# Kernel optimization log

Hardware: AMD Instinct MI355X
Metric: run time of the kernel (lower is better)

The kernel has to match this reference:

```python
import jax, jax.numpy as jnp
import numpy as np

B, L, D_MODEL = 2, 1024, 1024
EXPAND = 2
D_INNER = EXPAND * D_MODEL      # 2048
D_STATE = 16
D_CONV = 4
DT_RANK = D_MODEL // 16         # 64


def setup_inputs() -> dict:
    key = jax.random.key(0)
    ks = jax.random.split(key, 8)
    s = 0.02
    x = jax.random.normal(ks[0], (B, L, D_MODEL), jnp.float32)
    W_in = (jax.random.normal(ks[1], (D_MODEL, 2 * D_INNER), jnp.float32) * s)
    conv_w = jax.random.normal(ks[2], (D_INNER, 1, D_CONV), jnp.float32) * 0.2  # depthwise kernel (O,I/g,K)
    conv_b = jnp.zeros((D_INNER,), jnp.float32)
    W_xproj = jax.random.normal(ks[3], (D_INNER, DT_RANK + 2 * D_STATE), jnp.float32) * s
    W_dt = jax.random.normal(ks[4], (DT_RANK, D_INNER), jnp.float32) * (DT_RANK ** -0.5)
    b_dt = jnp.full((D_INNER,), -4.6, jnp.float32)  # softplus^{-1}(~0.01), mamba-style dt init
    A_log = jnp.log(jnp.broadcast_to(jnp.arange(1, D_STATE + 1, dtype=jnp.float32), (D_INNER, D_STATE)))
    D_skip = jnp.ones((D_INNER,), jnp.float32)
    W_out = jax.random.normal(ks[5], (D_INNER, D_MODEL), jnp.float32) * s
    return dict(x=x, W_in=W_in, conv_w=conv_w, conv_b=conv_b, W_xproj=W_xproj,
                W_dt=W_dt, b_dt=b_dt, A_log=A_log, D_skip=D_skip, W_out=W_out)


def _mamba(x, W_in, conv_w, conv_b, W_xproj, W_dt, b_dt, A_log, D_skip, W_out):
    b, l, _ = x.shape
    # input projection and gate split
    xz = jnp.einsum('bld,de->ble', x, W_in)            # (B, L, 2*d_inner)
    x_in, z = jnp.split(xz, 2, axis=-1)                # each (B, L, d_inner)
    # causal depthwise conv1d + SiLU
    xt = jnp.transpose(x_in, (0, 2, 1))                # (B, d_inner, L)
    xt = jnp.pad(xt, ((0, 0), (0, 0), (D_CONV - 1, 0)))
    conv = jax.lax.conv_general_dilated(
        xt, conv_w, window_strides=(1,), padding='VALID',
        dimension_numbers=('NCH', 'OIH', 'NCH'), feature_group_count=D_INNER)
    conv = conv + conv_b[None, :, None]                # (B, d_inner, L)
    u = jax.nn.silu(jnp.transpose(conv, (0, 2, 1)))    # (B, L, d_inner)
    # input-dependent SSM parameters
    x_dbl = jnp.einsum('bld,de->ble', u, W_xproj)      # (B, L, dt_rank + 2*d_state)
    dt_lr = x_dbl[..., :DT_RANK]
    Bm = x_dbl[..., DT_RANK:DT_RANK + D_STATE]         # (B, L, d_state)
    Cm = x_dbl[..., DT_RANK + D_STATE:]                # (B, L, d_state)
    delta = jax.nn.softplus(jnp.einsum('blr,rd->bld', dt_lr, W_dt) + b_dt)  # (B, L, d_inner)
    A = -jnp.exp(A_log)                                # (d_inner, d_state)
    dA = jnp.exp(jnp.einsum('bld,dn->bldn', delta, A))           # (B, L, d_inner, d_state)
    dBu = (delta * u)[..., None] * Bm[:, :, None, :]              # (B, L, d_inner, d_state)
    # selective scan over time
    def step(h, inp):
        dA_t, dBu_t, C_t = inp
        h = dA_t * h + dBu_t                           # (B, d_inner, d_state)
        y_t = jnp.einsum('bdn,bn->bd', h, C_t)
        return h, y_t
    h0 = jnp.zeros((b, D_INNER, D_STATE), x.dtype)
    _, ys = jax.lax.scan(step, h0, (jnp.swapaxes(dA, 0, 1), jnp.swapaxes(dBu, 0, 1), jnp.swapaxes(Cm, 0, 1)))
    y = jnp.swapaxes(ys, 0, 1)                          # (B, L, d_inner)
    y = y + D_skip * u
    y = y * jax.nn.silu(z)
    out = jnp.einsum('bld,de->ble', y, W_out)           # (B, L, d_model)
    return out  # dropout is identity in eval mode


def reference(x, W_in, conv_w, conv_b, W_xproj, W_dt, b_dt, A_log, D_skip, W_out):
    return _mamba(x, W_in, conv_w, conv_b, W_xproj, W_dt, b_dt, A_log, D_skip, W_out)
```

## Files before the change

### kernel.cpp

```cpp
#include <hip/hip_runtime.h>
#include <cmath>

#define B_  2
#define L_  1024
#define DM  1024
#define DI  2048
#define DS  16
#define DR  64
#define NC  32
#define CL  (L_/NC)

typedef __attribute__((ext_vector_type(8))) short short8;
typedef __attribute__((ext_vector_type(4))) float f32x4;

static __device__ __forceinline__ ushort f2bf(float f) {
    union { float f; unsigned u; } c; c.f = f;
    unsigned u = c.u;
    return (ushort)((u + 0x7fffu + ((u >> 16) & 1u)) >> 16);
}
static __device__ __forceinline__ float bf2f(ushort h) {
    union { unsigned u; float f; } c; c.u = ((unsigned)h) << 16;
    return c.f;
}

static __device__ __forceinline__ float softplus_f(float v) {
    return (v > 20.f) ? v : log1pf(__expf(v));
}

static __device__ void bt_body(const float* __restrict__ in,
                               ushort* __restrict__ oh, ushort* __restrict__ ol,
                               int K, int N, int Npad, int bx, int by,
                               float (*t)[33])
{
    const int tid = threadIdx.x;
    const int tx = tid & 31, ty = tid >> 5;
    const int n0 = bx * 32, k0 = by * 32;
    #pragma unroll
    for (int i = 0; i < 4; ++i) {
        int k = k0 + ty * 4 + i, n = n0 + tx;
        t[ty * 4 + i][tx] = (n < N) ? in[(size_t)k * N + n] : 0.f;
    }
    __syncthreads();
    #pragma unroll
    for (int i = 0; i < 4; ++i) {
        int r = n0 + ty * 4 + i;
        int c = k0 + tx;
        if (r < Npad) {
            float v = t[tx][ty * 4 + i];
            ushort h = f2bf(v);
            oh[(size_t)r * K + c] = h;
            if (ol) ol[(size_t)r * K + c] = f2bf(v - bf2f(h));
        }
    }
}

__global__ __launch_bounds__(256) void prep_all(
    const float* __restrict__ x, const float* __restrict__ W_in,
    const float* __restrict__ W_xprj, const float* __restrict__ W_dt,
    const float* __restrict__ W_out,
    ushort* __restrict__ Xh, ushort* __restrict__ WIh,
    ushort* __restrict__ WXh, ushort* __restrict__ WXl,
    ushort* __restrict__ WDh, ushort* __restrict__ WDl,
    ushort* __restrict__ Woh)
{
    __shared__ float t[32][33];
    int blk = blockIdx.x;
    if (blk < 4096) {
        bt_body(W_in, WIh, nullptr, 1024, 4096, 4096, blk & 127, blk >> 7, t);
    } else if (blk < 4352) {
        int b2 = blk - 4096;
        bt_body(W_xprj, WXh, WXl, 2048, 96, 128, b2 & 3, b2 >> 2, t);
    } else if (blk < 4480) {
        int b2 = blk - 4352;
        bt_body(W_dt, WDh, WDl, 64, 2048, 2048, b2 & 63, b2 >> 6, t);
    } else if (blk < 5504) {
        int v = (blk - 4480) * 256 + threadIdx.x;
        int r  = v >> 7;
        int c8 = v & 127;
        const float* p = x + (size_t)r * DM + c8 * 8;
        float4 v0 = *(const float4*)p;
        float4 v1 = *(const float4*)(p + 4);
        float vv[8] = {v0.x, v0.y, v0.z, v0.w, v1.x, v1.y, v1.z, v1.w};
        unsigned h[4];
        #pragma unroll
        for (int j = 0; j < 4; ++j)
            h[j] = (unsigned)f2bf(vv[2*j]) | ((unsigned)f2bf(vv[2*j+1]) << 16);
        size_t o = (size_t)r * 1024 + c8 * 8;
        *(uint4*)&Xh[o] = make_uint4(h[0], h[1], h[2], h[3]);
    } else {
        int b2 = blk - 5504;
        bt_body(W_out, Woh, nullptr, 2048, 1024, 1024, b2 & 31, b2 >> 5, t);
    }
}

static __device__ __forceinline__ void stage_tile(
    ushort* lds, const ushort* __restrict__ g, int ld, int row0, int k0,
    int wid, int lane)
{
    #pragma unroll
    for (int it = 0; it < 2; ++it) {
        int o  = wid * 2048 + it * 1024;
        int ob = o + lane * 16;
        int a  = ob ^ (((ob >> 7) & 7) << 4);
        int row = a >> 6;
        int lc  = (a >> 4) & 3;
        const ushort* gp = g + (size_t)(row0 + row) * ld + k0 + lc * 8;
        __builtin_amdgcn_global_load_lds(
            (const __attribute__((address_space(1))) void*)gp,
            (__attribute__((address_space(3))) void*)((char*)lds + o),
            16, 0, 0);
    }
}

static __device__ __forceinline__ void stage_tile64(
    ushort* lds, const ushort* __restrict__ g, int ld, int row0, int k0,
    int wid, int lane)
{
    int o  = wid * 1024;
    int ob = o + lane * 16;
    int a  = ob ^ (((ob >> 7) & 7) << 4);
    int row = a >> 6;
    int lc  = (a >> 4) & 3;
    const ushort* gp = g + (size_t)(row0 + row) * ld + k0 + lc * 8;
    __builtin_amdgcn_global_load_lds(
        (const __attribute__((address_space(1))) void*)gp,
        (__attribute__((address_space(3))) void*)((char*)lds + o),
        16, 0, 0);
}

static __device__ __forceinline__ short8 frag(const ushort* lds, int row, int fq) {
    int a = row * 64 + fq * 16;
    int b = a ^ (((a >> 7) & 7) << 4);
    return *(const short8*)((const char*)lds + b);
}

template<int TERMS>
static __device__ __forceinline__ void stage_all(
    ushort* buf, const ushort* Ah, const ushort* Bh, const ushort* Bl,
    int lda, int ldb, int bm, int bn, int k, int wid, int lane)
{
    stage_tile(buf,        Ah, lda, bm, k, wid, lane);
    stage_tile(buf + 4096, Bh, ldb, bn, k, wid, lane);
    if (TERMS == 2) stage_tile(buf + 8192, Bl, ldb, bn, k, wid, lane);
}

template<int TERMS>
static __device__ __forceinline__ void compute_tile(
    const ushort* buf, int wr, int wc, int fr, int fq, f32x4 acc[4][4])
{
    const ushort* sAh = buf;
    const ushort* sBh = buf + 4096;
    const ushort* sBl = buf + 8192;
    short8 a_h[4], b_h[4], b_l[4];
    #pragma unroll
    for (int m = 0; m < 4; ++m)
        a_h[m] = frag(sAh, wr + m * 16 + fr, fq);
    #pragma unroll
    for (int n = 0; n < 4; ++n) {
        b_h[n] = frag(sBh, wc + n * 16 + fr, fq);
        if (TERMS == 2) b_l[n] = frag(sBl, wc + n * 16 + fr, fq);
    }
    #pragma unroll
    for (int m = 0; m < 4; ++m)
        #pragma unroll
        for (int n = 0; n < 4; ++n) {
            acc[m][n] = __builtin_amdgcn_mfma_f32_16x16x32_bf16(a_h[m], b_h[n], acc[m][n], 0, 0, 0);
            if (TERMS == 2)
                acc[m][n] = __builtin_amdgcn_mfma_f32_16x16x32_bf16(a_h[m], b_l[n], acc[m][n], 0, 0, 0);
        }
}

template<int TERMS, int EPI>
__global__ __launch_bounds__(256) void gemm_bt(
    const ushort* __restrict__ Ah,
    const ushort* __restrict__ Bh, const ushort* __restrict__ Bl,
    float* __restrict__ C, ushort* __restrict__ oh,
    const float* __restrict__ bvec,
    int M, int N, int lda, int ldb, int ldc, int kspl)
{
    constexpr int TILE = TERMS == 1 ? 8192 : 12288;
    __shared__ ushort sm[2 * TILE];

    const int tid = threadIdx.x, wid = tid >> 6, lane = tid & 63;
    const int bm = blockIdx.y * 128, bn = blockIdx.x * 128;
    const int kb = blockIdx.z * kspl;
    const int wr = (wid >> 1) * 64, wc = (wid & 1) * 64;
    const int fr = lane & 15, fq = lane >> 4;

    f32x4 acc[4][4] = {};

    stage_all<TERMS>(sm, Ah, Bh, Bl, lda, ldb, bm, bn, kb, wid, lane);
    __syncthreads();
    int cur = 0;
    for (int k0 = 32; k0 < kspl; k0 += 32) {
        ushort* nbuf       = cur ? sm : sm + TILE;
        const ushort* cbuf = cur ? sm + TILE : sm;
        stage_all<TERMS>(nbuf, Ah, Bh, Bl, lda, ldb, bm, bn, kb + k0, wid, lane);
        compute_tile<TERMS>(cbuf, wr, wc, fr, fq, acc);
        __syncthreads();
        cur ^= 1;
    }
    compute_tile<TERMS>(cur ? sm + TILE : sm, wr, wc, fr, fq, acc);

    #pragma unroll
    for (int m = 0; m < 4; ++m) {
        int rbase = bm + wr + m * 16 + fq * 4;
        #pragma unroll
        for (int n = 0; n < 4; ++n) {
            int col = bn + wc + n * 16 + fr;
            if (col >= N) continue;
            if (EPI == 0) {
                #pragma unroll
                for (int j = 0; j < 4; ++j)
                    C[((size_t)blockIdx.z * M + rbase + j) * ldc + col] = acc[m][n][j];
            } else if (EPI == 1) {
                float bb = bvec[col];
                #pragma unroll
                for (int j = 0; j < 4; ++j)
                    oh[(size_t)(rbase + j) * ldc + col] =
                        f2bf(softplus_f(acc[m][n][j] + bb));
            } else {
                if (col < 2048) {
                    #pragma unroll
                    for (int j = 0; j < 4; ++j)
                        C[(size_t)(rbase + j) * 2048 + col] = acc[m][n][j];
                } else {
                    #pragma unroll
                    for (int j = 0; j < 4; ++j)
                        oh[(size_t)(rbase + j) * 2048 + (col - 2048)] =
                            f2bf(acc[m][n][j]);
                }
            }
        }
    }
}

__global__ __launch_bounds__(256) void gemm_out64(
    const ushort* __restrict__ Ah, const ushort* __restrict__ Bh,
    float* __restrict__ C, int K, int lda, int ldb, int ldc)
{
    __shared__ ushort sm[12288];
    const int tid = threadIdx.x, wid = tid >> 6, lane = tid & 63;
    const int bm = blockIdx.y * 128, bn = blockIdx.x * 64;
    const int wr = (wid >> 1) * 64, wc = (wid & 1) * 32;
    const int fr = lane & 15, fq = lane >> 4;

    f32x4 acc[4][2] = {};

    stage_tile  (sm,        Ah, lda, bm, 0, wid, lane);
    stage_tile64(sm + 4096, Bh, ldb, bn, 0, wid, lane);
    __syncthreads();
    int cur = 0;
    for (int k0 = 32; k0 < K; k0 += 32) {
        ushort* nbuf       = cur ? sm : sm + 6144;
        const ushort* cbuf = cur ? sm + 6144 : sm;
        stage_tile  (nbuf,        Ah, lda, bm, k0, wid, lane);
        stage_tile64(nbuf + 4096, Bh, ldb, bn, k0, wid, lane);
        {
            short8 a_h[4], b_h[2];
            #pragma unroll
            for (int m = 0; m < 4; ++m)
                a_h[m] = frag(cbuf, wr + m * 16 + fr, fq);
            #pragma unroll
            for (int n = 0; n < 2; ++n)
                b_h[n] = frag(cbuf + 4096, wc + n * 16 + fr, fq);
            #pragma unroll
            for (int m = 0; m < 4; ++m)
                #pragma unroll
                for (int n = 0; n < 2; ++n)
                    acc[m][n] = __builtin_amdgcn_mfma_f32_16x16x32_bf16(a_h[m], b_h[n], acc[m][n], 0, 0, 0);
        }
        __syncthreads();
        cur ^= 1;
    }
    {
        const ushort* cbuf = cur ? sm + 6144 : sm;
        short8 a_h[4], b_h[2];
        #pragma unroll
        for (int m = 0; m < 4; ++m)
            a_h[m] = frag(cbuf, wr + m * 16 + fr, fq);
        #pragma unroll
        for (int n = 0; n < 2; ++n)
            b_h[n] = frag(cbuf + 4096, wc + n * 16 + fr, fq);
        #pragma unroll
        for (int m = 0; m < 4; ++m)
            #pragma unroll
            for (int n = 0; n < 2; ++n)
                acc[m][n] = __builtin_amdgcn_mfma_f32_16x16x32_bf16(a_h[m], b_h[n], acc[m][n], 0, 0, 0);
    }

    #pragma unroll
    for (int m = 0; m < 4; ++m) {
        int rbase = bm + wr + m * 16 + fq * 4;
        #pragma unroll
        for (int n = 0; n < 2; ++n) {
            int col = bn + wc + n * 16 + fr;
            #pragma unroll
            for (int j = 0; j < 4; ++j)
                C[(size_t)(rbase + j) * ldc + col] = acc[m][n][j];
        }
    }
}

__global__ __launch_bounds__(256) void reduce_xproj(
    const float* __restrict__ p, float* __restrict__ xdbl,
    ushort* __restrict__ DTh)
{
    int i = blockIdx.x * 256 + threadIdx.x;
    if (i >= 2048 * 96) return;
    float s = 0.f;
    #pragma unroll
    for (int c = 0; c < 16; ++c) s += p[i + (size_t)c * (2048 * 96)];
    xdbl[i] = s;
    int row = i / 96, col = i - row * 96;
    if (col < 64) DTh[row * 64 + col] = f2bf(s);
}

__global__ __launch_bounds__(256) void conv_silu(
    const float* __restrict__ xin, const float* __restrict__ w,
    const float* __restrict__ bias, ushort* __restrict__ uh)
{
    int idx = blockIdx.x * 256 + threadIdx.x;
    if (idx >= B_ * L_ * DI) return;
    int d  = idx & (DI - 1);
    int bl = idx >> 11;
    int l  = bl & (L_ - 1);

    const float w0 = w[d * 4 + 0], w1 = w[d * 4 + 1];
    const float w2 = w[d * 4 + 2], w3 = w[d * 4 + 3];
    float s = bias[d];
    size_t base = (size_t)bl * 2048 + d;
    if (l >= 3) s = fmaf(w0, xin[base - 3 * 2048], s);
    if (l >= 2) s = fmaf(w1, xin[base - 2 * 2048], s);
    if (l >= 1) s = fmaf(w2, xin[base - 1 * 2048], s);
    s = fmaf(w3, xin[base], s);
    float v = s / (1.f + __expf(-s));
    uh[idx] = f2bf(v);
}

__global__ __launch_bounds__(256) void scan_partial(
    const ushort* __restrict__ Dh, const ushort* __restrict__ uh,
    const float* __restrict__ xdbl, const float* __restrict__ A_log,
    float* __restrict__ sA, float* __restrict__ sH)
{
    __shared__ float Bs[CL][16];
    const int tid  = threadIdx.x;
    const int dblk = blockIdx.x & 7;
    const int c    = (blockIdx.x >> 3) & (NC - 1);
    const int b    = blockIdx.x >> 8;
    const int d    = dblk * 256 + tid;
    const int bl0  = b * L_ + c * CL;

    for (int i = tid; i < CL * 16; i += 256) {
        int t = i >> 4, n = i & 15;
        Bs[t][n] = xdbl[(size_t)(bl0 + t) * 96 + DR + n];
    }
    __syncthreads();

    float Adn[16];
    #pragma unroll
    for (int q = 0; q < 4; ++q) {
        float4 al = *(const float4*)&A_log[d * DS + q * 4];
        Adn[q * 4 + 0] = -__expf(al.x);
        Adn[q * 4 + 1] = -__expf(al.y);
        Adn[q * 4 + 2] = -__expf(al.z);
        Adn[q * 4 + 3] = -__expf(al.w);
    }
    float h[16];
    #pragma unroll
    for (int n = 0; n < 16; ++n) h[n] = 0.f;
    float S = 0.f;

    size_t pd = (size_t)bl0 * DI + d;
    for (int t = 0; t < CL; ++t) {
        float dv = bf2f(Dh[pd]);
        float uv = bf2f(uh[pd]);
        float du = dv * uv;
        S += dv;
        float Bv[16];
        *(float4*)&Bv[0]  = *(const float4*)&Bs[t][0];
        *(float4*)&Bv[4]  = *(const float4*)&Bs[t][4];
        *(float4*)&Bv[8]  = *(const float4*)&Bs[t][8];
        *(float4*)&Bv[12] = *(const float4*)&Bs[t][12];
        #pragma unroll
        for (int n = 0; n < 16; ++n) {
            float dA = __expf(dv * Adn[n]);
            h[n] = fmaf(dA, h[n], du * Bv[n]);
        }
        pd += DI;
    }

    size_t o = (((size_t)c * B_ + b) * DI + d) * DS;
    float aP[16], hh[16];
    #pragma unroll
    for (int n = 0; n < 16; ++n) { aP[n] = __expf(S * Adn[n]); hh[n] = h[n]; }
    #pragma unroll
    for (int q = 0; q < 4; ++q) {
        *(float4*)&sA[o + q * 4] = *(float4*)&aP[q * 4];
        *(float4*)&sH[o + q * 4] = *(float4*)&hh[q * 4];
    }
}

__global__ __launch_bounds__(256) void scan_combine(
    const float* __restrict__ sA, const float* __restrict__ sH,
    float* __restrict__ hinit)
{
    int idx = blockIdx.x * 256 + threadIdx.x;
    int n = idx & 15;
    int d = (idx >> 4) & (DI - 1);
    int b = idx >> 15;
    float h = 0.f;
    #pragma unroll
    for (int c = 0; c < NC; ++c) {
        size_t o = (((size_t)c * B_ + b) * DI + d) * DS + n;
        hinit[o] = h;
        h = fmaf(sA[o], h, sH[o]);
    }
}

__global__ __launch_bounds__(256) void scan_final(
    const ushort* __restrict__ Dh, const ushort* __restrict__ uh,
    const float* __restrict__ xdbl, const ushort* __restrict__ Zh,
    const float* __restrict__ A_log, const float* __restrict__ D_skip,
    const float* __restrict__ hinit, ushort* __restrict__ yh)
{
    __shared__ float Bs[CL][16];
    __shared__ float Cs[CL][16];
    const int tid  = threadIdx.x;
    const int dblk = blockIdx.x & 7;
    const int c    = (blockIdx.x >> 3) & (NC - 1);
    const int b    = blockIdx.x >> 8;
    const int d    = dblk * 256 + tid;
    const int bl0  = b * L_ + c * CL;

    for (int i = tid; i < CL * 16; i += 256) {
        int t = i >> 4, n = i & 15;
        size_t px = (size_t)(bl0 + t) * 96 + DR + n;
        Bs[t][n] = xdbl[px];
        Cs[t][n] = xdbl[px + DS];
    }
    __syncthreads();

    float Adn[16];
    #pragma unroll
    for (int q = 0; q < 4; ++q) {
        float4 al = *(const float4*)&A_log[d * DS + q * 4];
        Adn[q * 4 + 0] = -__expf(al.x);
        Adn[q * 4 + 1] = -__expf(al.y);
        Adn[q * 4 + 2] = -__expf(al.z);
        Adn[q * 4 + 3] = -__expf(al.w);
    }
    const float Dd = D_skip[d];

    float h[16];
    size_t o = (((size_t)c * B_ + b) * DI + d) * DS;
    #pragma unroll
    for (int q = 0; q < 4; ++q)
        *(float4*)&h[q * 4] = *(const float4*)&hinit[o + q * 4];

    size_t pd = (size_t)bl0 * DI + d;
    for (int t = 0; t < CL; ++t) {
        float dv = bf2f(Dh[pd]);
        float uv = bf2f(uh[pd]);
        float du = dv * uv;
        float Bv[16], Cv[16];
        *(float4*)&Bv[0]  = *(const float4*)&Bs[t][0];
        *(float4*)&Bv[4]  = *(const float4*)&Bs[t][4];
        *(float4*)&Bv[8]  = *(const float4*)&Bs[t][8];
        *(float4*)&Bv[12] = *(const float4*)&Bs[t][12];
        *(float4*)&Cv[0]  = *(const float4*)&Cs[t][0];
        *(float4*)&Cv[4]  = *(const float4*)&Cs[t][4];
        *(float4*)&Cv[8]  = *(const float4*)&Cs[t][8];
        *(float4*)&Cv[12] = *(const float4*)&Cs[t][12];
        float acc = 0.f;
        #pragma unroll
        for (int n = 0; n < 16; ++n) {
            float dA = __expf(dv * Adn[n]);
            h[n] = fmaf(dA, h[n], du * Bv[n]);
            acc = fmaf(h[n], Cv[n], acc);
        }
        float zv = bf2f(Zh[pd]);
        float yv = acc + Dd * uv;
        yv *= zv / (1.f + __expf(-zv));
        yh[pd] = f2bf(yv);
        pd += DI;
    }
}

extern "C" void kernel_launch(void* const* d_in, const int* in_sizes, int n_in,
                              void* d_out, int out_size, void* d_ws, size_t ws_size,
                              hipStream_t stream)
{
    const float* x      = (const float*)d_in[0];
    const float* W_in   = (const float*)d_in[1];
    const float* conv_w = (const float*)d_in[2];
    const float* conv_b = (const float*)d_in[3];
    const float* W_xprj = (const float*)d_in[4];
    const float* W_dt   = (const float*)d_in[5];
    const float* b_dt   = (const float*)d_in[6];
    const float* A_log  = (const float*)d_in[7];
    const float* D_skip = (const float*)d_in[8];
    const float* W_out  = (const float*)d_in[9];
    float* out = (float*)d_out;

    char* ws = (char*)d_ws;
    float*  Xin   = (float*)(ws + 0);
    ushort* Zh    = (ushort*)(ws + 16777216);
    ushort* Dh    = (ushort*)(ws + 33554432);
    float*  xdbl  = (float*)(ws + 50331648);
    ushort* Woh   = (ushort*)(ws + 51118080);
    ushort* Xh    = (ushort*)(ws + 57409536);
    float*  parts = (float*)(ws + 57409536);
    ushort* WIh   = (ushort*)(ws + 65798144);
    float*  sA    = (float*)(ws + 57409536);
    float*  sH    = (float*)(ws + 65798144);
    float*  hin   = (float*)(ws + 74186752);
    ushort* Yh    = (ushort*)(ws + 57409536);
    ushort* Uh    = (ushort*)(ws + 82575360);
    ushort* WXh   = (ushort*)(ws + 99352576);
    ushort* WXl   = (ushort*)(ws + 99876864);
    ushort* DTh   = (ushort*)(ws + 100401152);
    ushort* WDh   = (ushort*)(ws + 100914176);
    ushort* WDl   = (ushort*)(ws + 101170688);

    dim3 blk(256);
    const int M = B_ * L_;

    prep_all<<<dim3(7552), blk, 0, stream>>>(
        x, W_in, W_xprj, W_dt, W_out, Xh, WIh, WXh, WXl, WDh, WDl, Woh);

    gemm_bt<1, 2><<<dim3(32, 16, 1), blk, 0, stream>>>(
        Xh, WIh, nullptr, Xin, Zh, nullptr,
        M, 4096, DM, DM, 2048, DM);

    conv_silu<<<dim3((B_ * L_ * DI) / 256), blk, 0, stream>>>(Xin, conv_w, conv_b, Uh);

    gemm_bt<2, 0><<<dim3(1, 16, 16), blk, 0, stream>>>(
        Uh, WXh, WXl, parts, nullptr, nullptr,
        M, 96, DI, DI, 96, 128);
    reduce_xproj<<<dim3(768), blk, 0, stream>>>(parts, xdbl, DTh);

    gemm_bt<2, 1><<<dim3(16, 16, 1), blk, 0, stream>>>(
        DTh, WDh, WDl, nullptr, Dh, b_dt,
        M, DI, DR, DR, DI, DR);

    scan_partial<<<dim3(B_ * NC * 8), blk, 0, stream>>>(
        Dh, Uh, xdbl, A_log, sA, sH);
    scan_combine<<<dim3((B_ * DI * DS) / 256), blk, 0, stream>>>(sA, sH, hin);
    scan_final<<<dim3(B_ * NC * 8), blk, 0, stream>>>(
        Dh, Uh, xdbl, Zh, A_log, D_skip, hin, Yh);

    gemm_out64<<<dim3(DM / 64, M / 128), blk, 0, stream>>>(
        Yh, Woh, out, DI, DI, DI, DM);
}
```

Measured before the change: 180.1 us.

## Fuse all pipeline stages into one cooperative persistent kernel with grid syncs

Merges the GEMMs, conv, reduction, chunked scan and output GEMM into a single cooperative kernel that loops over logical blocks and separates stages with grid.sync, and keeps separate kernels as a fallback. This removes eight kernel launches and their gaps. In exchange the fused kernel uses one shared buffer sized for the largest stage, which can lower occupancy, it is capped at 512 blocks, and it pays for grid-wide barriers and the host-side occupancy and attribute queries on every call.

After: 202.8 us. 1.13x slower.

```diff
diff --git a/kernel.cpp b/kernel.cpp
--- a/kernel.cpp
+++ b/kernel.cpp
@@ -1,5 +1,8 @@
 #include <hip/hip_runtime.h>
+#include <hip/hip_cooperative_groups.h>
 #include <cmath>
+
+namespace cg = cooperative_groups;
 
 #define B_  2
 #define L_  1024
@@ -171,22 +174,20 @@
 }
 
 template<int TERMS, int EPI>
-__global__ __launch_bounds__(256) void gemm_bt(
-    const ushort* __restrict__ Ah,
+static __device__ void dev_gemm(
+    ushort* sm, const ushort* __restrict__ Ah,
     const ushort* __restrict__ Bh, const ushort* __restrict__ Bl,
     float* __restrict__ C, ushort* __restrict__ oh,
     const float* __restrict__ bvec,
-    int M, int N, int lda, int ldb, int ldc, int kspl)
+    int M, int N, int lda, int ldb, int ldc, int kspl,
+    int bm, int bn, int kb, int zi)
 {
     constexpr int TILE = TERMS == 1 ? 8192 : 12288;
-    __shared__ ushort sm[2 * TILE];
-
     const int tid = threadIdx.x, wid = tid >> 6, lane = tid & 63;
-    const int bm = blockIdx.y * 128, bn = blockIdx.x * 128;
-    const int kb = blockIdx.z * kspl;
     const int wr = (wid >> 1) * 64, wc = (wid & 1) * 64;
     const int fr = lane & 15, fq = lane >> 4;
 
+    __syncthreads();
     f32x4 acc[4][4] = {};
 
     stage_all<TERMS>(sm, Ah, Bh, Bl, lda, ldb, bm, bn, kb, wid, lane);
@@ -212,7 +213,7 @@
             if (EPI == 0) {
                 #pragma unroll
                 for (int j = 0; j < 4; ++j)
-                    C[((size_t)blockIdx.z * M + rbase + j) * ldc + col] = acc[m][n][j];
+                    C[((size_t)zi * M + rbase + j) * ldc + col] = acc[m][n][j];
             } else if (EPI == 1) {
                 float bb = bvec[col];
                 #pragma unroll
@@ -235,16 +236,15 @@
     }
 }
 
-__global__ __launch_bounds__(256) void gemm_out64(
-    const ushort* __restrict__ Ah, const ushort* __restrict__ Bh,
-    float* __restrict__ C, int K, int lda, int ldb, int ldc)
-{
-    __shared__ ushort sm[12288];
+static __device__ void dev_gemm_out(
+    ushort* sm, const ushort* __restrict__ Ah, const ushort* __restrict__ Bh,
+    float* __restrict__ C, int K, int lda, int ldb, int ldc, int bm, int bn)
+{
     const int tid = threadIdx.x, wid = tid >> 6, lane = tid & 63;
-    const int bm = blockIdx.y * 128, bn = blockIdx.x * 64;
     const int wr = (wid >> 1) * 64, wc = (wid & 1) * 32;
     const int fr = lane & 15, fq = lane >> 4;
 
+    __syncthreads();
     f32x4 acc[4][2] = {};
 
     stage_tile  (sm,        Ah, lda, bm, 0, wid, lane);
@@ -302,30 +302,241 @@
     }
 }
 
-__global__ __launch_bounds__(256) void reduce_xproj(
-    const float* __restrict__ p, float* __restrict__ xdbl,
-    ushort* __restrict__ DTh)
-{
-    int i = blockIdx.x * 256 + threadIdx.x;
-    if (i >= 2048 * 96) return;
-    float s = 0.f;
-    #pragma unroll
-    for (int c = 0; c < 16; ++c) s += p[i + (size_t)c * (2048 * 96)];
-    xdbl[i] = s;
-    int row = i / 96, col = i - row * 96;
-    if (col < 64) DTh[row * 64 + col] = f2bf(s);
-}
-
-__global__ __launch_bounds__(256) void conv_silu(
-    const float* __restrict__ xin, const float* __restrict__ w,
-    const float* __restrict__ bias, ushort* __restrict__ uh)
+static __device__ void dev_scanA(
+    float* Bs, const ushort* __restrict__ Dh, const ushort* __restrict__ uh,
+    const float* __restrict__ xdbl, const float* __restrict__ A_log,
+    float* __restrict__ sA, float* __restrict__ sH, int blk)
+{
+    const int tid  = threadIdx.x;
+    const int dblk = blk & 7;
+    const int c    = (blk >> 3) & (NC - 1);
+    const int b    = blk >> 8;
+    const int d    = dblk * 256 + tid;
+    const int bl0  = b * L_ + c * CL;
+
+    __syncthreads();
+    for (int i = tid; i < CL * 16; i += 256) {
+        int t = i >> 4, n = i & 15;
+        Bs[t * 16 + n] = xdbl[(size_t)(bl0 + t) * 96 + DR + n];
+    }
+    __syncthreads();
+
+    float Adn[16];
+    #pragma unroll
+    for (int q = 0; q < 4; ++q) {
+        float4 al = *(const float4*)&A_log[d * DS + q * 4];
+        Adn[q * 4 + 0] = -__expf(al.x);
+        Adn[q * 4 + 1] = -__expf(al.y);
+        Adn[q * 4 + 2] = -__expf(al.z);
+        Adn[q * 4 + 3] = -__expf(al.w);
+    }
+    float h[16];
+    #pragma unroll
+    for (int n = 0; n < 16; ++n) h[n] = 0.f;
+    float S = 0.f;
+
+    size_t pd = (size_t)bl0 * DI + d;
+    for (int t = 0; t < CL; ++t) {
+        float dv = bf2f(Dh[pd]);
+        float uv = bf2f(uh[pd]);
+        float du = dv * uv;
+        S += dv;
+        float Bv[16];
+        #pragma unroll
+        for (int q = 0; q < 4; ++q)
+            *(float4*)&Bv[q * 4] = *(const float4*)&Bs[t * 16 + q * 4];
+        #pragma unroll
+        for (int n = 0; n < 16; ++n) {
+            float dA = __expf(dv * Adn[n]);
+            h[n] = fmaf(dA, h[n], du * Bv[n]);
+        }
+        pd += DI;
+    }
+
+    size_t o = (((size_t)c * B_ + b) * DI + d) * DS;
+    float aP[16];
+    #pragma unroll
+    for (int n = 0; n < 16; ++n) aP[n] = __expf(S * Adn[n]);
+    #pragma unroll
+    for (int q = 0; q < 4; ++q) {
+        *(float4*)&sA[o + q * 4] = *(float4*)&aP[q * 4];
+        *(float4*)&sH[o + q * 4] = *(float4*)&h[q * 4];
+    }
+}
+
+static __device__ void dev_scanC(
+    float* Bs, float* Cs, const ushort* __restrict__ Dh,
+    const ushort* __restrict__ uh, const float* __restrict__ xdbl,
+    const ushort* __restrict__ Zh, const float* __restrict__ A_log,
+    const float* __restrict__ D_skip, const float* __restrict__ hinit,
+    ushort* __restrict__ yh, int blk)
+{
+    const int tid  = threadIdx.x;
+    const int dblk = blk & 7;
+    const int c    = (blk >> 3) & (NC - 1);
+    const int b    = blk >> 8;
+    const int d    = dblk * 256 + tid;
+    const int bl0  = b * L_ + c * CL;
+
+    __syncthreads();
+    for (int i = tid; i < CL * 16; i += 256) {
+        int t = i >> 4, n = i & 15;
+        size_t px = (size_t)(bl0 + t) * 96 + DR + n;
+        Bs[t * 16 + n] = xdbl[px];
+        Cs[t * 16 + n] = xdbl[px + DS];
+    }
+    __syncthreads();
+
+    float Adn[16];
+    #pragma unroll
+    for (int q = 0; q < 4; ++q) {
+        float4 al = *(const float4*)&A_log[d * DS + q * 4];
+        Adn[q * 4 + 0] = -__expf(al.x);
+        Adn[q * 4 + 1] = -__expf(al.y);
+        Adn[q * 4 + 2] = -__expf(al.z);
+        Adn[q * 4 + 3] = -__expf(al.w);
+    }
+    const float Dd = D_skip[d];
+
+    float h[16];
+    size_t o = (((size_t)c * B_ + b) * DI + d) * DS;
+    #pragma unroll
+    for (int q = 0; q < 4; ++q)
+        *(float4*)&h[q * 4] = *(const float4*)&hinit[o + q * 4];
+
+    size_t pd = (size_t)bl0 * DI + d;
+    for (int t = 0; t < CL; ++t) {
+        float dv = bf2f(Dh[pd]);
+        float uv = bf2f(uh[pd]);
+        float du = dv * uv;
+        float Bv[16], Cv[16];
+        #pragma unroll
+        for (int q = 0; q < 4; ++q) {
+            *(float4*)&Bv[q * 4] = *(const float4*)&Bs[t * 16 + q * 4];
+            *(float4*)&Cv[q * 4] = *(const float4*)&Cs[t * 16 + q * 4];
+        }
+        float acc = 0.f;
+        #pragma unroll
+        for (int n = 0; n < 16; ++n) {
+            float dA = __expf(dv * Adn[n]);
+            h[n] = fmaf(dA, h[n], du * Bv[n]);
+            acc = fmaf(h[n], Cv[n], acc);
+        }
+        float zv = bf2f(Zh[pd]);
+        float yv = acc + Dd * uv;
+        yv *= zv / (1.f + __expf(-zv));
+        yh[pd] = f2bf(yv);
+        pd += DI;
+    }
+}
+
+__global__ __launch_bounds__(256) void mega(
+    const float* conv_w, const float* conv_b, const float* b_dt,
+    const float* A_log, const float* D_skip,
+    const ushort* Xh, const ushort* WIh,
+    const ushort* WXh, const ushort* WXl,
+    const ushort* WDh, const ushort* WDl, const ushort* Woh,
+    float* Xin, ushort* Zh, ushort* Dh, float* xdbl, ushort* DTh,
+    float* parts, ushort* Uh, float* sA, float* sH, float* hin,
+    ushort* Yh, float* out)
+{
+    cg::grid_group grid = cg::this_grid();
+    __shared__ ushort sm[24576];
+    const int blk = blockIdx.x;
+    const int tid = threadIdx.x;
+    const int G   = gridDim.x;
+
+    for (int lb = blk; lb < 512; lb += G)
+        dev_gemm<1, 2>(sm, Xh, WIh, nullptr, Xin, Zh, nullptr,
+                       2048, 4096, DM, DM, 2048, DM,
+                       (lb >> 5) * 128, (lb & 31) * 128, 0, 0);
+    grid.sync();
+
+    for (int idx = blk * 256 + tid; idx < B_ * L_ * DI; idx += G * 256) {
+        int d  = idx & (DI - 1);
+        int bl = idx >> 11;
+        int l  = bl & (L_ - 1);
+        const float w0 = conv_w[d * 4 + 0], w1 = conv_w[d * 4 + 1];
+        const float w2 = conv_w[d * 4 + 2], w3 = conv_w[d * 4 + 3];
+        float s = conv_b[d];
+        size_t base = (size_t)bl * 2048 + d;
+        if (l >= 3) s = fmaf(w0, Xin[base - 3 * 2048], s);
+        if (l >= 2) s = fmaf(w1, Xin[base - 2 * 2048], s);
+        if (l >= 1) s = fmaf(w2, Xin[base - 1 * 2048], s);
+        s = fmaf(w3, Xin[base], s);
+        float v = s / (1.f + __expf(-s));
+        Uh[idx] = f2bf(v);
+    }
+    grid.sync();
+
+    for (int lb = blk; lb < 256; lb += G)
+        dev_gemm<2, 0>(sm, Uh, WXh, WXl, parts, nullptr, nullptr,
+                       2048, 96, DI, DI, 96, 128,
+                       (lb >> 4) * 128, 0, (lb & 15) * 128, lb & 15);
+    grid.sync();
+
+    for (int i = blk * 256 + tid; i < 2048 * 96; i += G * 256) {
+        float s = 0.f;
+        #pragma unroll
+        for (int c = 0; c < 16; ++c) s += parts[i + (size_t)c * (2048 * 96)];
+        xdbl[i] = s;
+        int row = i / 96, col = i - row * 96;
+        if (col < 64) DTh[row * 64 + col] = f2bf(s);
+    }
+    grid.sync();
+
+    for (int lb = blk; lb < 256; lb += G)
+        dev_gemm<2, 1>(sm, DTh, WDh, WDl, nullptr, Dh, b_dt,
+                       2048, DI, DR, DR, DI, DR,
+                       (lb >> 4) * 128, (lb & 15) * 128, 0, 0);
+    grid.sync();
+
+    for (int lb = blk; lb < 512; lb += G)
+        dev_scanA((float*)sm, Dh, Uh, xdbl, A_log, sA, sH, lb);
+    grid.sync();
+
+    for (int lb = blk; lb < 256; lb += G) {
+        int idx = lb * 256 + tid;
+        int n = idx & 15;
+        int d = (idx >> 4) & (DI - 1);
+        int b = idx >> 15;
+        float h = 0.f;
+        #pragma unroll
+        for (int c = 0; c < NC; ++c) {
+            size_t o = (((size_t)c * B_ + b) * DI + d) * DS + n;
+            hin[o] = h;
+            h = fmaf(sA[o], h, sH[o]);
+        }
+    }
+    grid.sync();
+
+    for (int lb = blk; lb < 512; lb += G)
+        dev_scanC((float*)sm, (float*)sm + 512, Dh, Uh, xdbl, Zh, A_log,
+                  D_skip, hin, Yh, lb);
+    grid.sync();
+
+    for (int lb = blk; lb < 256; lb += G)
+        dev_gemm_out(sm, Yh, Woh, out, DI, DI, DI, DM,
+                     (lb >> 4) * 128, (lb & 15) * 64);
+}
+
+__global__ __launch_bounds__(256) void k_gemm1(
+    const ushort* Xh, const ushort* WIh, float* Xin, ushort* Zh)
+{
+    __shared__ ushort sm[16384];
+    dev_gemm<1, 2>(sm, Xh, WIh, nullptr, Xin, Zh, nullptr,
+                   2048, 4096, DM, DM, 2048, DM,
+                   blockIdx.y * 128, blockIdx.x * 128, 0, 0);
+}
+
+__global__ __launch_bounds__(256) void k_conv(
+    const float* xin, const float* w, const float* bias, ushort* uh)
 {
     int idx = blockIdx.x * 256 + threadIdx.x;
     if (idx >= B_ * L_ * DI) return;
     int d  = idx & (DI - 1);
     int bl = idx >> 11;
     int l  = bl & (L_ - 1);
-
     const float w0 = w[d * 4 + 0], w1 = w[d * 4 + 1];
     const float w2 = w[d * 4 + 2], w3 = w[d * 4 + 3];
     float s = bias[d];
@@ -338,72 +549,48 @@
     uh[idx] = f2bf(v);
 }
 
-__global__ __launch_bounds__(256) void scan_partial(
-    const ushort* __restrict__ Dh, const ushort* __restrict__ uh,
-    const float* __restrict__ xdbl, const float* __restrict__ A_log,
-    float* __restrict__ sA, float* __restrict__ sH)
-{
-    __shared__ float Bs[CL][16];
-    const int tid  = threadIdx.x;
-    const int dblk = blockIdx.x & 7;
-    const int c    = (blockIdx.x >> 3) & (NC - 1);
-    const int b    = blockIdx.x >> 8;
-    const int d    = dblk * 256 + tid;
-    const int bl0  = b * L_ + c * CL;
-
-    for (int i = tid; i < CL * 16; i += 256) {
-        int t = i >> 4, n = i & 15;
-        Bs[t][n] = xdbl[(size_t)(bl0 + t) * 96 + DR + n];
-    }
-    __syncthreads();
-
-    float Adn[16];
-    #pragma unroll
-    for (int q = 0; q < 4; ++q) {
-        float4 al = *(const float4*)&A_log[d * DS + q * 4];
-        Adn[q * 4 + 0] = -__expf(al.x);
-        Adn[q * 4 + 1] = -__expf(al.y);
-        Adn[q * 4 + 2] = -__expf(al.z);
-        Adn[q * 4 + 3] = -__expf(al.w);
-    }
-    float h[16];
-    #pragma unroll
-    for (int n = 0; n < 16; ++n) h[n] = 0.f;
-    float S = 0.f;
-
-    size_t pd = (size_t)bl0 * DI + d;
-    for (int t = 0; t < CL; ++t) {
-        float dv = bf2f(Dh[pd]);
-        float uv = bf2f(uh[pd]);
-        float du = dv * uv;
-        S += dv;
-        float Bv[16];
-        *(float4*)&Bv[0]  = *(const float4*)&Bs[t][0];
-        *(float4*)&Bv[4]  = *(const float4*)&Bs[t][4];
-        *(float4*)&Bv[8]  = *(const float4*)&Bs[t][8];
-        *(float4*)&Bv[12] = *(const float4*)&Bs[t][12];
-        #pragma unroll
-        for (int n = 0; n < 16; ++n) {
-            float dA = __expf(dv * Adn[n]);
-            h[n] = fmaf(dA, h[n], du * Bv[n]);
-        }
-        pd += DI;
-    }
-
-    size_t o = (((size_t)c * B_ + b) * DI + d) * DS;
-    float aP[16], hh[16];
-    #pragma unroll
-    for (int n = 0; n < 16; ++n) { aP[n] = __expf(S * Adn[n]); hh[n] = h[n]; }
-    #pragma unroll
-    for (int q = 0; q < 4; ++q) {
-        *(float4*)&sA[o + q * 4] = *(float4*)&aP[q * 4];
-        *(float4*)&sH[o + q * 4] = *(float4*)&hh[q * 4];
-    }
-}
-
-__global__ __launch_bounds__(256) void scan_combine(
-    const float* __restrict__ sA, const float* __restrict__ sH,
-    float* __restrict__ hinit)
+__global__ __launch_bounds__(256) void k_gemmX(
+    const ushort* Uh, const ushort* WXh, const ushort* WXl, float* parts)
+{
+    __shared__ ushort sm[24576];
+    dev_gemm<2, 0>(sm, Uh, WXh, WXl, parts, nullptr, nullptr,
+                   2048, 96, DI, DI, 96, 128,
+                   blockIdx.y * 128, 0, blockIdx.z * 128, blockIdx.z);
+}
+
+__global__ __launch_bounds__(256) void k_reduce(
+    const float* p, float* xdbl, ushort* DTh)
+{
+    int i = blockIdx.x * 256 + threadIdx.x;
+    if (i >= 2048 * 96) return;
+    float s = 0.f;
+    #pragma unroll
+    for (int c = 0; c < 16; ++c) s += p[i + (size_t)c * (2048 * 96)];
+    xdbl[i] = s;
+    int row = i / 96, col = i - row * 96;
+    if (col < 64) DTh[row * 64 + col] = f2bf(s);
+}
+
+__global__ __launch_bounds__(256) void k_gemmD(
+    const ushort* DTh, const ushort* WDh, const ushort* WDl, ushort* Dh,
+    const float* b_dt)
+{
+    __shared__ ushort sm[24576];
+    dev_gemm<2, 1>(sm, DTh, WDh, WDl, nullptr, Dh, b_dt,
+                   2048, DI, DR, DR, DI, DR,
+                   blockIdx.y * 128, blockIdx.x * 128, 0, 0);
+}
+
+__global__ __launch_bounds__(256) void k_scanA(
+    const ushort* Dh, const ushort* Uh, const float* xdbl, const float* A_log,
+    float* sA, float* sH)
+{
+    __shared__ float Bs[512];
+    dev_scanA(Bs, Dh, Uh, xdbl, A_log, sA, sH, blockIdx.x);
+}
+
+__global__ __launch_bounds__(256) void k_comb(
+    const float* sA, const float* sH, float* hin)
 {
     int idx = blockIdx.x * 256 + threadIdx.x;
     int n = idx & 15;
@@ -413,78 +600,26 @@
     #pragma unroll
     for (int c = 0; c < NC; ++c) {
         size_t o = (((size_t)c * B_ + b) * DI + d) * DS + n;
-        hinit[o] = h;
+        hin[o] = h;
         h = fmaf(sA[o], h, sH[o]);
     }
 }
 
-__global__ __launch_bounds__(256) void scan_final(
-    const ushort* __restrict__ Dh, const ushort* __restrict__ uh,
-    const float* __restrict__ xdbl, const ushort* __restrict__ Zh,
-    const float* __restrict__ A_log, const float* __restrict__ D_skip,
-    const float* __restrict__ hinit, ushort* __restrict__ yh)
-{
-    __shared__ float Bs[CL][16];
-    __shared__ float Cs[CL][16];
-    const int tid  = threadIdx.x;
-    const int dblk = blockIdx.x & 7;
-    const int c    = (blockIdx.x >> 3) & (NC - 1);
-    const int b    = blockIdx.x >> 8;
-    const int d    = dblk * 256 + tid;
-    const int bl0  = b * L_ + c * CL;
-
-    for (int i = tid; i < CL * 16; i += 256) {
-        int t = i >> 4, n = i & 15;
-        size_t px = (size_t)(bl0 + t) * 96 + DR + n;
-        Bs[t][n] = xdbl[px];
-        Cs[t][n] = xdbl[px + DS];
-    }
-    __syncthreads();
-
-    float Adn[16];
-    #pragma unroll
-    for (int q = 0; q < 4; ++q) {
-        float4 al = *(const float4*)&A_log[d * DS + q * 4];
-        Adn[q * 4 + 0] = -__expf(al.x);
-        Adn[q * 4 + 1] = -__expf(al.y);
-        Adn[q * 4 + 2] = -__expf(al.z);
-        Adn[q * 4 + 3] = -__expf(al.w);
-    }
-    const float Dd = D_skip[d];
-
-    float h[16];
-    size_t o = (((size_t)c * B_ + b) * DI + d) * DS;
-    #pragma unroll
-    for (int q = 0; q < 4; ++q)
-        *(float4*)&h[q * 4] = *(const float4*)&hinit[o + q * 4];
-
-    size_t pd = (size_t)bl0 * DI + d;
-    for (int t = 0; t < CL; ++t) {
-        float dv = bf2f(Dh[pd]);
-        float uv = bf2f(uh[pd]);
-        float du = dv * uv;
-        float Bv[16], Cv[16];
-        *(float4*)&Bv[0]  = *(const float4*)&Bs[t][0];
-        *(float4*)&Bv[4]  = *(const float4*)&Bs[t][4];
-        *(float4*)&Bv[8]  = *(const float4*)&Bs[t][8];
-        *(float4*)&Bv[12] = *(const float4*)&Bs[t][12];
-        *(float4*)&Cv[0]  = *(const float4*)&Cs[t][0];
-        *(float4*)&Cv[4]  = *(const float4*)&Cs[t][4];
-        *(float4*)&Cv[8]  = *(const float4*)&Cs[t][8];
-        *(float4*)&Cv[12] = *(const float4*)&Cs[t][12];
-        float acc = 0.f;
-        #pragma unroll
-        for (int n = 0; n < 16; ++n) {
-            float dA = __expf(dv * Adn[n]);
-            h[n] = fmaf(dA, h[n], du * Bv[n]);
-            acc = fmaf(h[n], Cv[n], acc);
-        }
-        float zv = bf2f(Zh[pd]);
-        float yv = acc + Dd * uv;
-        yv *= zv / (1.f + __expf(-zv));
-        yh[pd] = f2bf(yv);
-        pd += DI;
-    }
+__global__ __launch_bounds__(256) void k_scanC(
+    const ushort* Dh, const ushort* Uh, const float* xdbl, const ushort* Zh,
+    const float* A_log, const float* D_skip, const float* hin, ushort* Yh)
+{
+    __shared__ float BsCs[1024];
+    dev_scanC(BsCs, BsCs + 512, Dh, Uh, xdbl, Zh, A_log, D_skip, hin, Yh,
+              blockIdx.x);
+}
+
+__global__ __launch_bounds__(256) void k_out(
+    const ushort* Yh, const ushort* Woh, float* out)
+{
+    __shared__ ushort sm[12288];
+    dev_gemm_out(sm, Yh, Woh, out, DI, DI, DI, DM,
+                 blockIdx.y * 128, blockIdx.x * 64);
 }
 
 extern "C" void kernel_launch(void* const* d_in, const int* in_sizes, int n_in,
@@ -524,32 +659,37 @@
     ushort* WDl   = (ushort*)(ws + 101170688);
 
     dim3 blk(256);
-    const int M = B_ * L_;
 
     prep_all<<<dim3(7552), blk, 0, stream>>>(
         x, W_in, W_xprj, W_dt, W_out, Xh, WIh, WXh, WXl, WDh, WDl, Woh);
 
-    gemm_bt<1, 2><<<dim3(32, 16, 1), blk, 0, stream>>>(
-        Xh, WIh, nullptr, Xin, Zh, nullptr,
-        M, 4096, DM, DM, 2048, DM);
-
-    conv_silu<<<dim3((B_ * L_ * DI) / 256), blk, 0, stream>>>(Xin, conv_w, conv_b, Uh);
-
-    gemm_bt<2, 0><<<dim3(1, 16, 16), blk, 0, stream>>>(
-        Uh, WXh, WXl, parts, nullptr, nullptr,
-        M, 96, DI, DI, 96, 128);
-    reduce_xproj<<<dim3(768), blk, 0, stream>>>(parts, xdbl, DTh);
-
-    gemm_bt<2, 1><<<dim3(16, 16, 1), blk, 0, stream>>>(
-        DTh, WDh, WDl, nullptr, Dh, b_dt,
-        M, DI, DR, DR, DI, DR);
-
-    scan_partial<<<dim3(B_ * NC * 8), blk, 0, stream>>>(
-        Dh, Uh, xdbl, A_log, sA, sH);
-    scan_combine<<<dim3((B_ * DI * DS) / 256), blk, 0, stream>>>(sA, sH, hin);
-    scan_final<<<dim3(B_ * NC * 8), blk, 0, stream>>>(
-        Dh, Uh, xdbl, Zh, A_log, D_skip, hin, Yh);
-
-    gemm_out64<<<dim3(DM / 64, M / 128), blk, 0, stream>>>(
-        Yh, Woh, out, DI, DI, DI, DM);
-}
+    int dev = 0;
+    hipGetDevice(&dev);
+    int coop = 0;
+    hipDeviceGetAttribute(&coop, hipDeviceAttributeCooperativeLaunch, dev);
+    int occ = 0;
+    hipOccupancyMaxActiveBlocksPerMultiprocessor(&occ, mega, 256, 0);
+    int grid = occ * 256;
+    if (grid > 512) grid = 512;
+
+    if (coop && grid >= 256) {
+        void* args[] = {
+            (void*)&conv_w, (void*)&conv_b, (void*)&b_dt, (void*)&A_log,
+            (void*)&D_skip, (void*)&Xh, (void*)&WIh, (void*)&WXh, (void*)&WXl,
+            (void*)&WDh, (void*)&WDl, (void*)&Woh, (void*)&Xin, (void*)&Zh,
+            (void*)&Dh, (void*)&xdbl, (void*)&DTh, (void*)&parts, (void*)&Uh,
+            (void*)&sA, (void*)&sH, (void*)&hin, (void*)&Yh, (void*)&out
+        };
+        hipLaunchCooperativeKernel((void*)mega, dim3(grid), blk, args, 0, stream);
+    } else {
+        k_gemm1<<<dim3(32, 16), blk, 0, stream>>>(Xh, WIh, Xin, Zh);
+        k_conv<<<dim3(16384), blk, 0, stream>>>(Xin, conv_w, conv_b, Uh);
+        k_gemmX<<<dim3(1, 16, 16), blk, 0, stream>>>(Uh, WXh, WXl, parts);
+        k_reduce<<<dim3(768), blk, 0, stream>>>(parts, xdbl, DTh);
+        k_gemmD<<<dim3(16, 16), blk, 0, stream>>>(DTh, WDh, WDl, Dh, b_dt);
+        k_scanA<<<dim3(512), blk, 0, stream>>>(Dh, Uh, xdbl, A_log, sA, sH);
+        k_comb<<<dim3(256), blk, 0, stream>>>(sA, sH, hin);
+        k_scanC<<<dim3(512), blk, 0, stream>>>(Dh, Uh, xdbl, Zh, A_log, D_skip, hin, Yh);
+        k_out<<<dim3(16, 16), blk, 0, stream>>>(Yh, Woh, out);
+    }
+}
```
